# Kernel tuning notes

Hardware: AMD Instinct MI355X
Metric: run time of the kernel (lower is better)

## Reference

```python
import jax, jax.numpy as jnp
import numpy as np

B, S, D_IN, D_OUT = 4, 2048, 2048, 8192


def setup_inputs() -> dict:
    key = jax.random.key(0)
    k1, k2 = jax.random.split(key)
    x = jax.random.normal(k1, (B, S, D_IN), dtype=jnp.float32)
    weight = jax.random.normal(k2, (D_OUT, D_IN), dtype=jnp.float32) * 0.02
    alpha = jnp.float32(1.0)
    bias = jnp.zeros((D_OUT,), dtype=jnp.float32)
    return {"x": x, "weight": weight, "alpha": alpha, "bias": bias}


def reference(x, weight, alpha, bias):
    # Ternary quantization: delta = 0.7 * mean(|w|); w_q in {-1,0,1} * alpha
    delta = 0.7 * jnp.mean(jnp.abs(weight))
    w_t = jnp.where(weight > delta, jnp.float32(1.0),
                    jnp.where(weight < -delta, jnp.float32(-1.0), jnp.float32(0.0)))
    w_q = w_t * alpha  # [out, in]
    # F.linear: x @ w_q^T + bias
    return jnp.einsum('bsd,od->bso', x, w_q) + bias
```

## Files before the change

kernel.cpp:

```cpp
#include <hip/hip_runtime.h>
#include <hip/hip_bf16.h>
#include <stdint.h>

typedef __attribute__((ext_vector_type(4))) int i32x4;
typedef __attribute__((ext_vector_type(16))) int i32x16;
typedef signed char s8;

#define M_TOT 8192
#define N_TOT 8192
#define K_TOT 2048
#define W_COUNT (N_TOT * K_TOT)
#define X_COUNT (M_TOT * K_TOT)

__global__ void tl_reduce(const float* __restrict__ w, const float* __restrict__ x,
                          double* __restrict__ wsum, float* __restrict__ xmax) {
    const int b = blockIdx.x;
    if (b < 1024) {
        const int tid = b * 256 + threadIdx.x;
        const float4* w4 = (const float4*)w;
        double s = 0.0;
        for (int i = tid; i < W_COUNT / 4; i += 1024 * 256) {
            float4 v = w4[i];
            s += (double)fabsf(v.x) + (double)fabsf(v.y) + (double)fabsf(v.z) + (double)fabsf(v.w);
        }
        #pragma unroll
        for (int off = 32; off > 0; off >>= 1) s += __shfl_down(s, off);
        __shared__ double red[4];
        if ((threadIdx.x & 63) == 0) red[threadIdx.x >> 6] = s;
        __syncthreads();
        if (threadIdx.x == 0) wsum[b] = (red[0] + red[1]) + (red[2] + red[3]);
    } else {
        const int tid = (b - 1024) * 256 + threadIdx.x;
        const float4* x4 = (const float4*)x;
        float m = 0.0f;
        for (int i = tid; i < X_COUNT / 4; i += 1024 * 256) {
            float4 v = x4[i];
            m = fmaxf(m, fmaxf(fmaxf(fabsf(v.x), fabsf(v.y)), fmaxf(fabsf(v.z), fabsf(v.w))));
        }
        #pragma unroll
        for (int off = 32; off > 0; off >>= 1) m = fmaxf(m, __shfl_down(m, off));
        __shared__ float redm[4];
        if ((threadIdx.x & 63) == 0) redm[threadIdx.x >> 6] = m;
        __syncthreads();
        if (threadIdx.x == 0) xmax[b - 1024] = fmaxf(fmaxf(redm[0], redm[1]), fmaxf(redm[2], redm[3]));
    }
}

__global__ void tl_finalize(const double* __restrict__ wsum, const float* __restrict__ xmax,
                            const float* __restrict__ alpha,
                            double* __restrict__ delta, float* __restrict__ qp) {
    const int t = threadIdx.x;
    double s = (wsum[t] + wsum[t + 256]) + (wsum[t + 512] + wsum[t + 768]);
    float m = fmaxf(fmaxf(xmax[t], xmax[t + 256]), fmaxf(xmax[t + 512], xmax[t + 768]));
    #pragma unroll
    for (int off = 32; off > 0; off >>= 1) {
        s += __shfl_down(s, off);
        m = fmaxf(m, __shfl_down(m, off));
    }
    __shared__ double rs[4];
    __shared__ float rm[4];
    if ((t & 63) == 0) { rs[t >> 6] = s; rm[t >> 6] = m; }
    __syncthreads();
    if (t == 0) {
        *delta = 0.7 * (((rs[0] + rs[1]) + (rs[2] + rs[3])) / (double)W_COUNT);
        float mm = fmaxf(fmaxf(rm[0], rm[1]), fmaxf(rm[2], rm[3]));
        qp[0] = 127.0f / mm;
        qp[1] = alpha[0] * (mm / 127.0f);
    }
}

__global__ void tl_tern_w(const float* __restrict__ w, const double* __restrict__ delta_p,
                          s8* __restrict__ wbF) {
    const double d = *delta_p;
    const int i = blockIdx.x * 256 + threadIdx.x;
    const int frag = i >> 6, lane = i & 63;
    const int n = (frag >> 6) * 32 + (lane & 31);
    const int k = (frag & 63) * 32 + (lane >> 5) * 16;
    const float* src = w + (size_t)n * K_TOT + k;
    union { s8 c[16]; i32x4 v; } o;
    #pragma unroll
    for (int j = 0; j < 16; j += 4) {
        float4 v = *(const float4*)(src + j);
        float f[4] = {v.x, v.y, v.z, v.w};
        #pragma unroll
        for (int r = 0; r < 4; ++r) {
            double wd = (double)f[r];
            o.c[j + r] = wd > d ? 1 : (wd < -d ? -1 : 0);
        }
    }
    *(i32x4*)(wbF + (size_t)i * 16) = o.v;
}

__global__ void tl_quant_x(const float* __restrict__ x, const float* __restrict__ qp,
                           s8* __restrict__ xb) {
    const float inv = qp[0];
    const int i = (blockIdx.x * 256 + threadIdx.x) * 16;
    union { s8 c[16]; i32x4 v; } o;
    #pragma unroll
    for (int j = 0; j < 16; j += 4) {
        float4 v = *(const float4*)(x + i + j);
        float f[4] = {v.x, v.y, v.z, v.w};
        #pragma unroll
        for (int r = 0; r < 4; ++r) {
            int q = (int)__builtin_rintf(f[r] * inv);
            q = q > 127 ? 127 : (q < -127 ? -127 : q);
            o.c[j + r] = (s8)q;
        }
    }
    *(i32x4*)(xb + i) = o.v;
}


#define SB    __builtin_amdgcn_sched_barrier(0)
#define BARR  __builtin_amdgcn_s_barrier()
#define LGKM4 asm volatile("s_waitcnt lgkmcnt(4)" ::: "memory")
#define LGKM0 asm volatile("s_waitcnt lgkmcnt(0)" ::: "memory")
#define VMW(N) asm volatile("s_waitcnt vmcnt(" #N ")" ::: "memory")
#define PRIO1 __builtin_amdgcn_s_setprio(1)
#define PRIO0 __builtin_amdgcn_s_setprio(0)

#define GLDS(SRC, DOFF) __builtin_amdgcn_global_load_lds(                      \
    (const __attribute__((address_space(1))) void*)(SRC),                      \
    (__attribute__((address_space(3))) void*)(lds + (DOFF)), 16, 0, 0)

#define RD_A4(AR, S, KK) do {                                                  \
    _Pragma("unroll") for (int m_ = 0; m_ < 4; ++m_)                           \
        AR[m_] = *(const i32x4*)(lds + (S) * 16384 + wrOff + m_ * 2048 +       \
                                 (lrd ^ ((KK) * 32)));                         \
} while (0)

#define LDB4(BX, BOFF) do {                                                    \
    BX[0] = *(const i32x4*)(bPtr + (BOFF));                                    \
    BX[1] = *(const i32x4*)(bPtr + (BOFF) + 1024);                             \
    BX[2] = *(const i32x4*)(bPtr + (BOFF) + 65536);                            \
    BX[3] = *(const i32x4*)(bPtr + (BOFF) + 65536 + 1024);                     \
} while (0)

#define MM8(AX, B0, B1) do {                                                   \
    _Pragma("unroll") for (int m_ = 0; m_ < 4; ++m_) {                         \
        acc[m_][0] = __builtin_amdgcn_mfma_i32_32x32x32_i8(AX[m_], B0, acc[m_][0], 0, 0, 0); \
        acc[m_][1] = __builtin_amdgcn_mfma_i32_32x32x32_i8(AX[m_], B1, acc[m_][1], 0, 0, 0); \
    }                                                                          \
} while (0)

#define STG_A(SS, KOFF) do {                                                   \
    GLDS(aSrc + (KOFF), (SS) * 16384 + L);                                     \
    GLDS(aSrc + (KOFF) + 262144, (SS) * 16384 + 8192 + L);                     \
} while (0)

#define KT(S, SN, SG, BCUR, BNXT, W1, W2, DOSTG, DOB, DONEXT) do {             \
    RD_A4(aO, S, 1);                                                           \
    if (DOB) { LDB4(BNXT, boff); }                                             \
    SB;                                                                        \
    if (DOSTG) { STG_A(SG, koff); }                                            \
    SB;                                                                        \
    W1; SB;                                                                    \
    LGKM4; SB;                                                                 \
    PRIO1; MM8(aE, BCUR[0], BCUR[2]); PRIO0; SB;                               \
    LGKM0; SB;                                                                 \
    W2; SB;                                                                    \
    BARR; SB;                                                                  \
    if (DONEXT) { RD_A4(aE, SN, 0); SB; }                                      \
    PRIO1; MM8(aO, BCUR[1], BCUR[3]); PRIO0; SB;                               \
    koff += 64; boff += 2048;                                                  \
} while (0)

__global__ __launch_bounds__(512, 2) void tl_gemm_i8(
    const s8* __restrict__ A, const s8* __restrict__ BmF,
    const float* __restrict__ qp, const float* __restrict__ bias,
    float* __restrict__ C) {
    __shared__ __attribute__((aligned(128))) char lds[49152];

    const int t = threadIdx.x;
    const int wid = t >> 6;
    const int l = t & 63;
    const int wr = wid >> 2;
    const int wc = wid & 3;

    const int bid = blockIdx.x;
    const int xc = bid & 7;
    const int j = bid >> 3;
    const int tm = xc * 4 + ((j >> 3) & 3);
    const int tn = (j >> 5) * 8 + (j & 7);
    const int row0 = tm * 256, col0 = tn * 256;

    const int L = t * 16;
    const int off = L ^ (((L >> 7) & 3) << 4);
    const int sr = off >> 6;
    const int kb = off & 63;
    const s8* aSrc = A + (size_t)(row0 + sr) * K_TOT + kb;

    const s8* bPtr = BmF + (size_t)((col0 >> 5) + wc * 2) * 65536 + l * 16;

    const int rl = l & 31, kg = l >> 5;
    const int lrd = rl * 64 + ((kg ^ ((rl >> 1) & 3)) << 4);
    const int wrOff = wr * 8192;

    i32x16 acc[4][2] = {};
    i32x4 aE[4], aO[4], bC[4], bN[4];

    STG_A(0, 0); SB;
    LDB4(bC, 0); SB;
    STG_A(1, 64); SB;
    VMW(6); SB;
    BARR; SB;
    RD_A4(aE, 0, 0); SB;

    int koff = 128;
    int boff = 2048;
    #pragma unroll 1
    for (int i = 0; i < 5; ++i) {
        KT(0, 1, 2, bC, bN, VMW(8), VMW(6), 1, 1, 1);
        KT(1, 2, 0, bN, bC, VMW(8), VMW(6), 1, 1, 1);
        KT(2, 0, 1, bC, bN, VMW(8), VMW(6), 1, 1, 1);
        KT(0, 1, 2, bN, bC, VMW(8), VMW(6), 1, 1, 1);
        KT(1, 2, 0, bC, bN, VMW(8), VMW(6), 1, 1, 1);
        KT(2, 0, 1, bN, bC, VMW(8), VMW(6), 1, 1, 1);
    }
    KT(0, 1, 0, bC, bN, VMW(6), VMW(4), 0, 1, 1);
    KT(1, 0, 0, bN, bC, VMW(0), (void)0, 0, 0, 0);

    const float osc = qp[1];
    #pragma unroll
    for (int m_ = 0; m_ < 4; ++m_) {
        const int crow = row0 + wr * 128 + m_ * 32 + kg * 4;
        #pragma unroll
        for (int n_ = 0; n_ < 2; ++n_) {
            const int ccol = col0 + wc * 64 + n_ * 32 + rl;
            const float bv = bias[ccol];
            #pragma unroll
            for (int r = 0; r < 16; ++r) {
                const int row = crow + (r & 3) + 8 * (r >> 2);
                C[(size_t)row * N_TOT + ccol] = (float)acc[m_][n_][r] * osc + bv;
            }
        }
    }
}

extern "C" void kernel_launch(void* const* d_in, const int* in_sizes, int n_in,
                              void* d_out, int out_size, void* d_ws, size_t ws_size,
                              hipStream_t stream) {
    const float* x     = (const float*)d_in[0];
    const float* wgt   = (const float*)d_in[1];
    const float* alpha = (const float*)d_in[2];
    const float* bias  = (const float*)d_in[3];
    float* out = (float*)d_out;

    char* ws = (char*)d_ws;
    double* wsum = (double*)ws;
    float* xmax  = (float*)(ws + 8192);
    double* delta = (double*)(ws + 12288);
    float* qp     = (float*)(ws + 12304);
    s8* xb = (s8*)(ws + 16384);
    s8* wb = (s8*)(ws + 16384 + (size_t)X_COUNT);

    tl_reduce<<<2048, 256, 0, stream>>>(wgt, x, wsum, xmax);
    tl_finalize<<<1, 256, 0, stream>>>(wsum, xmax, alpha, delta, qp);
    tl_tern_w<<<W_COUNT / (256 * 16), 256, 0, stream>>>(wgt, delta, wb);
    tl_quant_x<<<X_COUNT / (256 * 16), 256, 0, stream>>>(x, qp, xb);
    tl_gemm_i8<<<(M_TOT / 256) * (N_TOT / 256), 512, 0, stream>>>(xb, wb, qp, bias, out);
}
```

Before: 223.5 us.

## Triple-buffer B fragments and issue loads after first MFMA half

Rotates B register fragments through three buffers (X/Y/Z) so B is prefetched two K-steps ahead instead of one. Each K-step is reordered so the first MFMA half runs before the next global B loads and A LDS staging are issued, with a single vmcnt gate before the barrier. The aim is to hide global-load latency behind more MFMA work and simplify the wait structure. The cost is extra VGPRs for the third B buffer, which could cause spills or lower occupancy under the 512x2 launch bounds.

```diff
diff --git a/kernel.cpp b/kernel.cpp
--- a/kernel.cpp
+++ b/kernel.cpp
@@ -136,10 +136,12 @@
     BX[3] = *(const i32x4*)(bPtr + (BOFF) + 65536 + 1024);                     \
 } while (0)
 
-#define MM8(AX, B0, B1) do {                                                   \
+#define MMH(AR, BX, H) do {                                                    \
     _Pragma("unroll") for (int m_ = 0; m_ < 4; ++m_) {                         \
-        acc[m_][0] = __builtin_amdgcn_mfma_i32_32x32x32_i8(AX[m_], B0, acc[m_][0], 0, 0, 0); \
-        acc[m_][1] = __builtin_amdgcn_mfma_i32_32x32x32_i8(AX[m_], B1, acc[m_][1], 0, 0, 0); \
+        acc[m_][0] = __builtin_amdgcn_mfma_i32_32x32x32_i8(                    \
+            AR[m_], BX[0 + (H)], acc[m_][0], 0, 0, 0);                         \
+        acc[m_][1] = __builtin_amdgcn_mfma_i32_32x32x32_i8(                    \
+            AR[m_], BX[2 + (H)], acc[m_][1], 0, 0, 0);                         \
     }                                                                          \
 } while (0)
 
@@ -148,21 +150,16 @@
     GLDS(aSrc + (KOFF) + 262144, (SS) * 16384 + 8192 + L);                     \
 } while (0)
 
-#define KT(S, SN, SG, BCUR, BNXT, W1, W2, DOSTG, DOB, DONEXT) do {             \
+#define KT(S, SN, SG, BC, BN, KOFF, BOFF, DOISS, GATE, DONEXT) do {            \
     RD_A4(aO, S, 1);                                                           \
-    if (DOB) { LDB4(BNXT, boff); }                                             \
+    SB; LGKM4; SB;                                                             \
+    PRIO1; MMH(aE, BC, 0); PRIO0; SB;                                          \
+    if (DOISS) { LDB4(BN, BOFF); STG_A(SG, KOFF); }                            \
+    SB; LGKM0; SB;                                                             \
+    GATE; BARR; SB;                                                            \
+    if (DONEXT) RD_A4(aE, SN, 0);                                              \
     SB;                                                                        \
-    if (DOSTG) { STG_A(SG, koff); }                                            \
-    SB;                                                                        \
-    W1; SB;                                                                    \
-    LGKM4; SB;                                                                 \
-    PRIO1; MM8(aE, BCUR[0], BCUR[2]); PRIO0; SB;                               \
-    LGKM0; SB;                                                                 \
-    W2; SB;                                                                    \
-    BARR; SB;                                                                  \
-    if (DONEXT) { RD_A4(aE, SN, 0); SB; }                                      \
-    PRIO1; MM8(aO, BCUR[1], BCUR[3]); PRIO0; SB;                               \
-    koff += 64; boff += 2048;                                                  \
+    PRIO1; MMH(aO, BC, 1); PRIO0; SB;                                          \
 } while (0)
 
 __global__ __launch_bounds__(512, 2) void tl_gemm_i8(
@@ -197,28 +194,26 @@
     const int wrOff = wr * 8192;
 
     i32x16 acc[4][2] = {};
-    i32x4 aE[4], aO[4], bC[4], bN[4];
-
+    i32x4 aE[4], aO[4], bX[4], bY[4], bZ[4];
+
+    LDB4(bX, 0); SB;
     STG_A(0, 0); SB;
-    LDB4(bC, 0); SB;
     STG_A(1, 64); SB;
+    LDB4(bY, 2048); SB;
     VMW(6); SB;
     BARR; SB;
     RD_A4(aE, 0, 0); SB;
 
     int koff = 128;
-    int boff = 2048;
+    int boff = 4096;
     #pragma unroll 1
-    for (int i = 0; i < 5; ++i) {
-        KT(0, 1, 2, bC, bN, VMW(8), VMW(6), 1, 1, 1);
-        KT(1, 2, 0, bN, bC, VMW(8), VMW(6), 1, 1, 1);
-        KT(2, 0, 1, bC, bN, VMW(8), VMW(6), 1, 1, 1);
-        KT(0, 1, 2, bN, bC, VMW(8), VMW(6), 1, 1, 1);
-        KT(1, 2, 0, bC, bN, VMW(8), VMW(6), 1, 1, 1);
-        KT(2, 0, 1, bN, bC, VMW(8), VMW(6), 1, 1, 1);
-    }
-    KT(0, 1, 0, bC, bN, VMW(6), VMW(4), 0, 1, 1);
-    KT(1, 0, 0, bN, bC, VMW(0), (void)0, 0, 0, 0);
+    for (int i = 0; i < 10; ++i) {
+        KT(0, 1, 2, bX, bZ, koff, boff, 1, VMW(6), 1); koff += 64; boff += 2048;
+        KT(1, 2, 0, bY, bX, koff, boff, 1, VMW(6), 1); koff += 64; boff += 2048;
+        KT(2, 0, 1, bZ, bY, koff, boff, 1, VMW(6), 1); koff += 64; boff += 2048;
+    }
+    KT(0, 1, 0, bX, bZ, 0, 0, 0, VMW(0), 1);
+    KT(1, 0, 0, bY, bZ, 0, 0, 0, (void)0, 0);
 
     const float osc = qp[1];
     #pragma unroll
```

New measurement: 207.6 us. -7.1%, faster.
